# Kernel optimization log

Measured on AMD Instinct MI355X. Metric: run time of the kernel, lower is better.

## Reference

```python
import jax, jax.numpy as jnp
import numpy as np

B, L, DM = 8, 1024, 1024
H, P, N, K = 32, 64, 128, 4   # nheads, headdim, d_state, d_conv
DI = H * P                    # d_inner = expand * d_model = 2048
DXBC = DI + 2 * N             # conv channels = 2304
DINP = 2 * DI + 2 * N + H     # in_proj width = 4404
ED = 2048                     # embed_dim

def setup_inputs():
    key = jax.random.key(0)
    ks = jax.random.split(key, 10)
    s = lambda i, shape, scale=0.02: jax.random.normal(ks[i], shape, jnp.float32) * scale
    return {
        "bert_out": jax.random.normal(ks[0], (B, L, 1024), jnp.float32),
        "w_pb": s(1, (1024, DM)), "b_pb": jnp.zeros((DM,), jnp.float32),
        "w_in": s(2, (DM, DINP)),
        "conv_w": s(3, (DXBC, K), 0.2), "conv_b": jnp.zeros((DXBC,), jnp.float32),
        "dt_bias": jax.random.uniform(ks[4], (H,), jnp.float32, -4.0, 0.0),
        "A_log": jnp.log(jnp.arange(1, H + 1, dtype=jnp.float32)),
        "D": jnp.ones((H,), jnp.float32),
        "norm_w": jnp.ones((DI,), jnp.float32),
        "w_outp": s(5, (DI, DM)),
        "w_attn": s(6, (DM, 1)), "b_attn": jnp.zeros((1,), jnp.float32),
        "w_emb": s(7, (DM, ED)), "b_emb": jnp.zeros((ED,), jnp.float32),
    }

def reference(bert_out, w_pb, b_pb, w_in, conv_w, conv_b, dt_bias, A_log, D,
              norm_w, w_outp, w_attn, b_attn, w_emb, b_emb):
    x = bert_out @ w_pb + b_pb                          # [B,L,DM] proj_bert
    # ---- Mamba2 ----
    zxbcdt = x @ w_in                                   # [B,L,DINP]
    z, xBC, dt = jnp.split(zxbcdt, [DI, DI + DXBC], axis=-1)
    # causal depthwise conv1d (kernel K) + SiLU
    xp = jnp.pad(xBC, ((0, 0), (K - 1, 0), (0, 0)))
    xBC = sum(xp[:, k:k + L, :] * conv_w[:, k] for k in range(K)) + conv_b
    xBC = jax.nn.silu(xBC)
    xs, Bm, Cm = jnp.split(xBC, [DI, DI + N], axis=-1)  # [B,L,DI],[B,L,N],[B,L,N]
    xs = xs.reshape(B, L, H, P)
    dt = jax.nn.softplus(dt + dt_bias)                  # [B,L,H]
    dA = jnp.exp(dt * (-jnp.exp(A_log)))                # [B,L,H]
    def step(h, inp):
        dA_t, dt_t, B_t, C_t, x_t = inp
        h = h * dA_t[:, :, None, None] + jnp.einsum('bh,bn,bhp->bhpn', dt_t, B_t, x_t)
        return h, jnp.einsum('bhpn,bn->bhp', h, C_t)
    h0 = jnp.zeros((B, H, P, N), x.dtype)
    _, ys = jax.lax.scan(step, h0, (dA.transpose(1, 0, 2), dt.transpose(1, 0, 2),
                                    Bm.transpose(1, 0, 2), Cm.transpose(1, 0, 2),
                                    xs.transpose(1, 0, 2, 3)))
    y = ys.transpose(1, 0, 2, 3) + D[None, None, :, None] * xs   # skip term
    y = y.reshape(B, L, DI) * jax.nn.silu(z)                     # gated
    y = y * jax.lax.rsqrt(jnp.mean(y * y, axis=-1, keepdims=True) + 1e-5) * norm_w
    emb = y @ w_outp                                             # [B,L,DM]
    # ---- attention pooling ----
    w = jax.nn.softmax(emb @ w_attn + b_attn, axis=1)            # [B,L,1]
    pooled = (emb * w).sum(axis=1)                               # [B,DM]
    # dropout is identity in eval mode
    return pooled @ w_emb + b_emb                                # [B,ED]
```

## Files before the change

### kernel.cpp

```cpp
#include <hip/hip_runtime.h>
#include <hip/hip_bf16.h>
#include <math.h>

#define B_    8
#define L_    1024
#define DM_   1024
#define H_    32
#define P_    64
#define NS_   128
#define DI_   2048
#define DXBC_ 2304
#define DINP_ 4384
#define ED_   2048

typedef __attribute__((ext_vector_type(8))) short bf8_t;
typedef __attribute__((ext_vector_type(8))) unsigned short u16x8;
typedef __attribute__((ext_vector_type(4))) float f4_t;

__device__ __forceinline__ float silu_f(float x) { return x / (1.f + __expf(-x)); }

__device__ __forceinline__ unsigned short f2bf(float x) {
    unsigned u = __float_as_uint(x);
    unsigned r = u + 0x7fffu + ((u >> 16) & 1u);
    return (unsigned short)(r >> 16);
}
__device__ __forceinline__ float bf2f(unsigned short h) {
    return __uint_as_float(((unsigned)h) << 16);
}

__global__ __launch_bounds__(256) void convw_k(
    const float* __restrict__ W, unsigned short* __restrict__ hi,
    unsigned short* __restrict__ lo, int K, int N, int Npad)
{
    size_t e = (size_t)blockIdx.x * 256 + threadIdx.x;
    if (e >= (size_t)K * Npad) return;
    int n = (int)(e % Npad), k = (int)(e / Npad);
    float v = (n < N) ? W[(size_t)k * N + n] : 0.f;
    unsigned short h = f2bf(v);
    unsigned short l = f2bf(v - bf2f(h));
    int nt = n >> 7, r = n & 127, kt = k >> 5, c = k & 31;
    size_t dst = ((size_t)(nt * (K >> 5) + kt) << 12) + (r << 5) + c;
    hi[dst] = h; lo[dst] = l;
}

__global__ __launch_bounds__(256) void conva_k(
    const float* __restrict__ A, unsigned short* __restrict__ hi,
    unsigned short* __restrict__ lo, int M, int K)
{
    size_t e = (size_t)blockIdx.x * 256 + threadIdx.x;
    if (e >= (size_t)M * K) return;
    int k = (int)(e % K), m = (int)(e / K);
    float v = A[e];
    unsigned short h = f2bf(v);
    unsigned short l = f2bf(v - bf2f(h));
    int mt = m >> 7, r = m & 127, kt = k >> 5, c = k & 31;
    size_t dst = ((size_t)(mt * (K >> 5) + kt) << 12) + (r << 5) + c;
    hi[dst] = h; lo[dst] = l;
}

template<bool CHECK_N>
__global__ __launch_bounds__(256, 2) void bgemm_k(
    const unsigned short* __restrict__ Ahi, const unsigned short* __restrict__ Alo,
    const unsigned short* __restrict__ Whi, const unsigned short* __restrict__ Wlo,
    float* __restrict__ C, const float* __restrict__ bias, int N, int K, int ldc)
{
    __shared__ unsigned short Ah[128 * 40], Al[128 * 40];
    __shared__ unsigned short Bh[128 * 40], Bl[128 * 40];
    const int tid = threadIdx.x;
    const int m0 = blockIdx.y * 128, n0 = blockIdx.x * 128;
    const int lane = tid & 63;
    const int wv = tid >> 6;
    const int wr = wv >> 1, wc = wv & 1;
    const int l15 = lane & 15, l4 = lane >> 4;
    const int KT = K >> 5;

    f4_t acc[4][4];
#pragma unroll
    for (int i = 0; i < 4; i++)
#pragma unroll
        for (int j = 0; j < 4; j++) acc[i][j] = (f4_t){0.f, 0.f, 0.f, 0.f};

    const int trow = tid >> 1;
    const int tcol = (tid & 1) * 16;
    const int soff = trow * 40 + tcol;

    u16x8 rAh0, rAh1, rAl0, rAl1, rWh0, rWh1, rWl0, rWl1;
#define LOADKT(KTI) {                                                               \
        size_t aoff = (((size_t)(blockIdx.y * KT + (KTI))) << 12) + (trow << 5) + tcol; \
        size_t woff = (((size_t)(blockIdx.x * KT + (KTI))) << 12) + (trow << 5) + tcol; \
        rAh0 = *(const u16x8*)(Ahi + aoff); rAh1 = *(const u16x8*)(Ahi + aoff + 8); \
        rAl0 = *(const u16x8*)(Alo + aoff); rAl1 = *(const u16x8*)(Alo + aoff + 8); \
        rWh0 = *(const u16x8*)(Whi + woff); rWh1 = *(const u16x8*)(Whi + woff + 8); \
        rWl0 = *(const u16x8*)(Wlo + woff); rWl1 = *(const u16x8*)(Wlo + woff + 8); }

    LOADKT(0);
    for (int kt = 0; kt < KT; ++kt) {
        __syncthreads();
        *(u16x8*)&Ah[soff]     = rAh0;
        *(u16x8*)&Ah[soff + 8] = rAh1;
        *(u16x8*)&Al[soff]     = rAl0;
        *(u16x8*)&Al[soff + 8] = rAl1;
        *(u16x8*)&Bh[soff]     = rWh0;
        *(u16x8*)&Bh[soff + 8] = rWh1;
        *(u16x8*)&Bl[soff]     = rWl0;
        *(u16x8*)&Bl[soff + 8] = rWl1;
        __syncthreads();
        if (kt + 1 < KT) LOADKT(kt + 1);

        bf8_t afh[4], afl[4], bfh[4], bfl[4];
#pragma unroll
        for (int i = 0; i < 4; i++) {
            int off = (wr * 64 + i * 16 + l15) * 40 + l4 * 8;
            afh[i] = *(const bf8_t*)&Ah[off];
            afl[i] = *(const bf8_t*)&Al[off];
        }
#pragma unroll
        for (int j = 0; j < 4; j++) {
            int off = (wc * 64 + j * 16 + l15) * 40 + l4 * 8;
            bfh[j] = *(const bf8_t*)&Bh[off];
            bfl[j] = *(const bf8_t*)&Bl[off];
        }
#pragma unroll
        for (int i = 0; i < 4; i++)
#pragma unroll
            for (int j = 0; j < 4; j++) {
                acc[i][j] = __builtin_amdgcn_mfma_f32_16x16x32_bf16(afh[i], bfh[j], acc[i][j], 0, 0, 0);
                acc[i][j] = __builtin_amdgcn_mfma_f32_16x16x32_bf16(afl[i], bfh[j], acc[i][j], 0, 0, 0);
                acc[i][j] = __builtin_amdgcn_mfma_f32_16x16x32_bf16(afh[i], bfl[j], acc[i][j], 0, 0, 0);
            }
    }
#undef LOADKT

#pragma unroll
    for (int j = 0; j < 4; j++) {
        int col = n0 + wc * 64 + j * 16 + l15;
        bool ok = !CHECK_N || (col < N);
        float bv = 0.f;
        if (bias && ok) bv = bias[col];
        if (ok) {
#pragma unroll
            for (int i = 0; i < 4; i++) {
                int rbase = m0 + wr * 64 + i * 16 + l4 * 4;
#pragma unroll
                for (int r = 0; r < 4; r++)
                    C[(size_t)(rbase + r) * ldc + col] = acc[i][j][r] + bv;
            }
        }
    }
}

template<bool CHECK_N>
__global__ __launch_bounds__(256, 2) void sgemm_k(
    const float* __restrict__ A, const float* __restrict__ Bw,
    float* __restrict__ C, const float* __restrict__ bias,
    int M, int N, int K, int ldb, int ldc)
{
    __shared__ float As[16][128];
    __shared__ float Bs[16][128];
    const int tid = threadIdx.x;
    const int m0 = blockIdx.y * 128;
    const int n0 = blockIdx.x * 128;
    const int tx = tid & 15;
    const int ty = tid >> 4;
    const int arr = tid >> 1;
    const int acc_ = (tid & 1) * 8;
    const int bk = tid >> 5;
    const int bn = (tid & 31) * 4;

    float acc[8][8];
#pragma unroll
    for (int i = 0; i < 8; i++)
#pragma unroll
        for (int j = 0; j < 8; j++) acc[i][j] = 0.f;

    for (int k0 = 0; k0 < K; k0 += 16) {
        float4 a0 = *(const float4*)(A + (size_t)(m0 + arr) * K + k0 + acc_);
        float4 a1 = *(const float4*)(A + (size_t)(m0 + arr) * K + k0 + acc_ + 4);
        float4 b0, b1;
        if (!CHECK_N || (n0 + bn) < N) {
            b0 = *(const float4*)(Bw + (size_t)(k0 + bk) * ldb + n0 + bn);
            b1 = *(const float4*)(Bw + (size_t)(k0 + bk + 8) * ldb + n0 + bn);
        } else {
            b0 = make_float4(0.f, 0.f, 0.f, 0.f);
            b1 = make_float4(0.f, 0.f, 0.f, 0.f);
        }
        __syncthreads();
        As[acc_ + 0][arr] = a0.x; As[acc_ + 1][arr] = a0.y;
        As[acc_ + 2][arr] = a0.z; As[acc_ + 3][arr] = a0.w;
        As[acc_ + 4][arr] = a1.x; As[acc_ + 5][arr] = a1.y;
        As[acc_ + 6][arr] = a1.z; As[acc_ + 7][arr] = a1.w;
        *(float4*)&Bs[bk][bn]     = b0;
        *(float4*)&Bs[bk + 8][bn] = b1;
        __syncthreads();
#pragma unroll
        for (int kk = 0; kk < 16; kk++) {
            float4 av0 = *(const float4*)&As[kk][ty * 8];
            float4 av1 = *(const float4*)&As[kk][ty * 8 + 4];
            float4 bv0 = *(const float4*)&Bs[kk][tx * 4];
            float4 bv1 = *(const float4*)&Bs[kk][64 + tx * 4];
            float a_[8] = {av0.x, av0.y, av0.z, av0.w, av1.x, av1.y, av1.z, av1.w};
            float b_[8] = {bv0.x, bv0.y, bv0.z, bv0.w, bv1.x, bv1.y, bv1.z, bv1.w};
#pragma unroll
            for (int i = 0; i < 8; i++)
#pragma unroll
                for (int j = 0; j < 8; j++) acc[i][j] += a_[i] * b_[j];
        }
    }
    float4 bb0 = make_float4(0.f, 0.f, 0.f, 0.f), bb1 = bb0;
    if (bias) {
        if (!CHECK_N || (n0 + tx * 4) < N)      bb0 = *(const float4*)(bias + n0 + tx * 4);
        if (!CHECK_N || (n0 + 64 + tx * 4) < N) bb1 = *(const float4*)(bias + n0 + 64 + tx * 4);
    }
#pragma unroll
    for (int i = 0; i < 8; i++) {
        size_t row = (size_t)(m0 + ty * 8 + i) * ldc + n0;
        if (!CHECK_N || (n0 + tx * 4) < N) {
            float4 v = make_float4(acc[i][0] + bb0.x, acc[i][1] + bb0.y,
                                   acc[i][2] + bb0.z, acc[i][3] + bb0.w);
            *(float4*)(C + row + tx * 4) = v;
        }
        if (!CHECK_N || (n0 + 64 + tx * 4) < N) {
            float4 v = make_float4(acc[i][4] + bb1.x, acc[i][5] + bb1.y,
                                   acc[i][6] + bb1.z, acc[i][7] + bb1.w);
            *(float4*)(C + row + 64 + tx * 4) = v;
        }
    }
}

__global__ __launch_bounds__(256) void dt_k(
    const float* __restrict__ zx, const float* __restrict__ dt_bias,
    const float* __restrict__ A_log, float* __restrict__ dtp, float* __restrict__ dAb)
{
    int e = blockIdx.x * 256 + threadIdx.x;
    int l = e & 1023;
    int h = (e >> 10) & 31;
    int b = e >> 15;
    float dtr = zx[((size_t)b * L_ + l) * DINP_ + (DI_ + DXBC_) + h];
    float u = dtr + dt_bias[h];
    float sp = (u > 20.f) ? u : log1pf(__expf(u));
    float da = __expf(-__expf(A_log[h]) * sp);
    size_t o = ((size_t)b * H_ + h) * L_ + l;
    dtp[o] = sp;
    dAb[o] = da;
}

__global__ __launch_bounds__(256) void stash_k(const float* __restrict__ zx, float* __restrict__ stash)
{
    int e = blockIdx.x * 256 + threadIdx.x;
    int c = e % DXBC_;
    int r = e / DXBC_;
    int k = r % 3;
    int bc = r / 3;
    int chunk = bc & 7;
    int b = bc >> 3;
    int t = chunk * 128 - 3 + k;
    float v = 0.f;
    if (t >= 0) v = zx[((size_t)b * L_ + t) * DINP_ + DI_ + c];
    stash[e] = v;
}

__global__ __launch_bounds__(256) void conv_k(
    float* __restrict__ zx, const float* __restrict__ cw,
    const float* __restrict__ cb, const float* __restrict__ stash)
{
    int tid = threadIdx.x;
    int cblk = blockIdx.x;
    int chunk = blockIdx.y;
    int b = blockIdx.z;
    int c = cblk * 256 + tid;
    float4 w = *(const float4*)(cw + (size_t)c * 4);
    float bias = cb[c];
    const float* st = stash + ((size_t)(b * 8 + chunk) * 3) * DXBC_ + c;
    float x0 = st[0], x1 = st[DXBC_], x2 = st[2 * DXBC_];
    int t0 = chunk * 128;
    size_t base = ((size_t)b * L_ + t0) * DINP_ + DI_ + c;
#pragma unroll 4
    for (int t = 0; t < 128; t++) {
        float xt = zx[base + (size_t)t * DINP_];
        float a = w.x * x0 + w.y * x1 + w.z * x2 + w.w * xt + bias;
        a = a / (1.f + __expf(-a));
        zx[base + (size_t)t * DINP_] = a;
        x0 = x1; x1 = x2; x2 = xt;
    }
}

__global__ __launch_bounds__(1024, 1) void scan_k(
    const float* __restrict__ zx, const float* __restrict__ dtp,
    const float* __restrict__ dAb, const float* __restrict__ Dp,
    float* __restrict__ ys)
{
    int bh = blockIdx.x;
    int b = bh >> 5, h = bh & 31;
    int tid = threadIdx.x;
    int lane = tid & 63;
    int gu = __builtin_amdgcn_readfirstlane(tid >> 6);
    int nbase = gu * 8;
    __shared__ float ypart[8][16][64];
    __shared__ float bcs[8][256];
    __shared__ float xss[8][64];
    __shared__ float dtda[2][8];
    float hreg[8];
#pragma unroll
    for (int j = 0; j < 8; j++) hreg[j] = 0.f;
    float Dh = Dp[h];
    const float* dtrow = dtp + ((size_t)b * H_ + h) * L_;
    const float* darow = dAb + ((size_t)b * H_ + h) * L_;

    const int st_t = tid >> 7;
    const int st_j = (tid & 127) * 2;
    const int sx_t = tid >> 6;
    const int sx_ok = (sx_t < 8);

    {
        size_t row = ((size_t)b * L_ + st_t) * DINP_;
        float2 bc2 = *(const float2*)(zx + row + 2 * DI_ + st_j);
        *(float2*)&bcs[st_t][st_j] = bc2;
        if (sx_ok) {
            size_t rowx = ((size_t)b * L_ + sx_t) * DINP_;
            xss[sx_t][lane] = zx[rowx + DI_ + h * 64 + lane];
        }
        if (tid < 8)               dtda[0][tid] = dtrow[tid];
        else if (tid < 16)         dtda[1][tid - 8] = darow[tid - 8];
    }
    __syncthreads();

    float xout = 0.f;
    for (int c0 = 0; c0 < L_; c0 += 8) {
        float2 nbc; float nx = 0.f, nd = 0.f;
        const bool pf = (c0 + 8) < L_;
        if (pf) {
            size_t row = ((size_t)b * L_ + c0 + 8 + st_t) * DINP_;
            nbc = *(const float2*)(zx + row + 2 * DI_ + st_j);
            if (sx_ok) {
                size_t rowx = ((size_t)b * L_ + c0 + 8 + sx_t) * DINP_;
                nx = zx[rowx + DI_ + h * 64 + lane];
            }
            if (tid < 8)       nd = dtrow[c0 + 8 + tid];
            else if (tid < 16) nd = darow[c0 + 8 + tid - 8];
        }
#pragma unroll
        for (int tt = 0; tt < 8; ++tt) {
            float dtv = dtda[0][tt];
            float dav = dtda[1][tt];
            float xv  = xss[tt][lane];
            if (tt == gu) xout = xv;
            float4 b0  = *(const float4*)&bcs[tt][nbase];
            float4 b1  = *(const float4*)&bcs[tt][nbase + 4];
            float4 cv0 = *(const float4*)&bcs[tt][128 + nbase];
            float4 cv1 = *(const float4*)&bcs[tt][128 + nbase + 4];
            float u = dtv * xv;
            float ya = 0.f, yb = 0.f;
            hreg[0] = hreg[0] * dav + u * b0.x; ya += hreg[0] * cv0.x;
            hreg[1] = hreg[1] * dav + u * b0.y; yb += hreg[1] * cv0.y;
            hreg[2] = hreg[2] * dav + u * b0.z; ya += hreg[2] * cv0.z;
            hreg[3] = hreg[3] * dav + u * b0.w; yb += hreg[3] * cv0.w;
            hreg[4] = hreg[4] * dav + u * b1.x; ya += hreg[4] * cv1.x;
            hreg[5] = hreg[5] * dav + u * b1.y; yb += hreg[5] * cv1.y;
            hreg[6] = hreg[6] * dav + u * b1.z; ya += hreg[6] * cv1.z;
            hreg[7] = hreg[7] * dav + u * b1.w; yb += hreg[7] * cv1.w;
            ypart[tt][gu][lane] = ya + yb;
        }
        __syncthreads();
        if (gu < 8) {
            int t = c0 + gu;
            float v = 0.f;
#pragma unroll
            for (int w = 0; w < 16; w++) v += ypart[gu][w][lane];
            ys[((size_t)b * L_ + t) * DI_ + h * 64 + lane] = v + Dh * xout;
        }
        if (pf) {
            *(float2*)&bcs[st_t][st_j] = nbc;
            if (sx_ok) xss[sx_t][lane] = nx;
            if (tid < 8)       dtda[0][tid] = nd;
            else if (tid < 16) dtda[1][tid - 8] = nd;
        }
        __syncthreads();
    }
}

__global__ __launch_bounds__(256) void gate_norm_k(
    float* __restrict__ ys, const float* __restrict__ zx, const float* __restrict__ nw)
{
    int row = blockIdx.x;
    int tid = threadIdx.x;
    float* yr = ys + (size_t)row * DI_;
    const float* zr = zx + (size_t)row * DINP_;
    float4 v[2];
    float ss = 0.f;
#pragma unroll
    for (int i = 0; i < 2; i++) {
        int d = tid * 4 + i * 1024;
        float4 yv = *(const float4*)(yr + d);
        float4 zv = *(const float4*)(zr + d);
        v[i].x = yv.x * silu_f(zv.x);
        v[i].y = yv.y * silu_f(zv.y);
        v[i].z = yv.z * silu_f(zv.z);
        v[i].w = yv.w * silu_f(zv.w);
        ss += v[i].x * v[i].x + v[i].y * v[i].y + v[i].z * v[i].z + v[i].w * v[i].w;
    }
    __shared__ float red[256];
    red[tid] = ss;
    __syncthreads();
    for (int s = 128; s > 0; s >>= 1) {
        if (tid < s) red[tid] += red[tid + s];
        __syncthreads();
    }
    float scale = rsqrtf(red[0] / (float)DI_ + 1e-5f);
#pragma unroll
    for (int i = 0; i < 2; i++) {
        int d = tid * 4 + i * 1024;
        float4 nwv = *(const float4*)(nw + d);
        float4 o = make_float4(v[i].x * scale * nwv.x, v[i].y * scale * nwv.y,
                               v[i].z * scale * nwv.z, v[i].w * scale * nwv.w);
        *(float4*)(yr + d) = o;
    }
}

__global__ __launch_bounds__(256) void attnw_k(
    const float* __restrict__ emb, const float* __restrict__ wat,
    const float* __restrict__ batn, float* __restrict__ logits)
{
    int row = blockIdx.x * 4 + (threadIdx.x >> 6);
    int lane = threadIdx.x & 63;
    const float* er = emb + (size_t)row * DM_;
    float s = 0.f;
#pragma unroll
    for (int k = 0; k < 16; k++) s += er[lane + k * 64] * wat[lane + k * 64];
#pragma unroll
    for (int off = 32; off; off >>= 1) s += __shfl_down(s, off);
    if (lane == 0) logits[row] = s + batn[0];
}

__global__ __launch_bounds__(256) void softmax_k(
    const float* __restrict__ logits, float* __restrict__ wght, float* __restrict__ pooled)
{
    int b = blockIdx.x;
    int tid = threadIdx.x;
    __shared__ float red[256];
    float4 lv = *(const float4*)(logits + (size_t)b * L_ + tid * 4);
    float m = fmaxf(fmaxf(lv.x, lv.y), fmaxf(lv.z, lv.w));
    red[tid] = m;
    __syncthreads();
    for (int s = 128; s > 0; s >>= 1) {
        if (tid < s) red[tid] = fmaxf(red[tid], red[tid + s]);
        __syncthreads();
    }
    float bm = red[0];
    __syncthreads();
    float e0 = __expf(lv.x - bm), e1 = __expf(lv.y - bm);
    float e2 = __expf(lv.z - bm), e3 = __expf(lv.w - bm);
    red[tid] = e0 + e1 + e2 + e3;
    __syncthreads();
    for (int s = 128; s > 0; s >>= 1) {
        if (tid < s) red[tid] += red[tid + s];
        __syncthreads();
    }
    float inv = 1.f / red[0];
    *(float4*)(wght + (size_t)b * L_ + tid * 4) = make_float4(e0 * inv, e1 * inv, e2 * inv, e3 * inv);
    *(float4*)(pooled + (size_t)b * DM_ + tid * 4) = make_float4(0.f, 0.f, 0.f, 0.f);
}

__global__ __launch_bounds__(256) void pool_k(
    const float* __restrict__ emb, const float* __restrict__ wght, float* __restrict__ pooled)
{
    int b = blockIdx.x, dc = blockIdx.y, lc = blockIdx.z;
    int d = dc * 256 + threadIdx.x;
    const float* wr = wght + (size_t)b * L_ + lc * 64;
    float acc = 0.f;
#pragma unroll 4
    for (int lt = 0; lt < 64; lt++)
        acc += emb[((size_t)(b * L_ + lc * 64 + lt)) * DM_ + d] * wr[lt];
    atomicAdd(pooled + (size_t)b * DM_ + d, acc);
}

__global__ __launch_bounds__(256) void outp_k(
    const float* __restrict__ pooled, const float* __restrict__ wemb,
    const float* __restrict__ bemb, float* __restrict__ out)
{
    int ec = blockIdx.x, b = blockIdx.y;
    int tid = threadIdx.x;
    __shared__ float pl[DM_];
#pragma unroll
    for (int i = 0; i < 4; i++) pl[tid + i * 256] = pooled[(size_t)b * DM_ + tid + i * 256];
    __syncthreads();
    int e = ec * 256 + tid;
    float acc = bemb[e];
#pragma unroll 4
    for (int d = 0; d < DM_; d++) acc += pl[d] * wemb[(size_t)d * ED_ + e];
    out[(size_t)b * ED_ + e] = acc;
}

extern "C" void kernel_launch(void* const* d_in, const int* in_sizes, int n_in,
                              void* d_out, int out_size, void* d_ws, size_t ws_size,
                              hipStream_t stream)
{
    (void)in_sizes; (void)n_in; (void)out_size;
    const float* bert    = (const float*)d_in[0];
    const float* w_pb    = (const float*)d_in[1];
    const float* b_pb    = (const float*)d_in[2];
    const float* w_in    = (const float*)d_in[3];
    const float* conv_w  = (const float*)d_in[4];
    const float* conv_b  = (const float*)d_in[5];
    const float* dt_bias = (const float*)d_in[6];
    const float* A_log   = (const float*)d_in[7];
    const float* Dp      = (const float*)d_in[8];
    const float* norm_w  = (const float*)d_in[9];
    const float* w_outp  = (const float*)d_in[10];
    const float* w_attn  = (const float*)d_in[11];
    const float* b_attn  = (const float*)d_in[12];
    const float* w_emb   = (const float*)d_in[13];
    const float* b_emb   = (const float*)d_in[14];
    float* out = (float*)d_out;

    float* ws     = (float*)d_ws;
    float* zx     = ws;
    float* ys     = zx  + (size_t)8192 * 4384;
    float* xe     = ys  + (size_t)8192 * 2048;
    float* dtp    = xe  + (size_t)8192 * 1024;
    float* dAb    = dtp + 262144;
    float* stash  = dAb + 262144;
    float* logits = stash + 442368;
    float* wght   = logits + 8192;
    float* pooled = wght + 8192;
    float* fend   = pooled + 8192;

    size_t wpb_n = (size_t)8  * 32 * 4096;
    size_t win_n = (size_t)35 * 32 * 4096;
    size_t wop_n = (size_t)8  * 64 * 4096;
    size_t aT_n  = (size_t)64 * 32 * 4096;
    size_t ysT_n = (size_t)64 * 64 * 4096;
    unsigned short* wpb_h = (unsigned short*)ys;
    unsigned short* wpb_l = wpb_h + wpb_n;
    unsigned short* win_h = wpb_l + wpb_n;
    unsigned short* win_l = win_h + win_n;
    unsigned short* aT_h  = win_l + win_n;
    unsigned short* aT_l  = aT_h + aT_n;
    unsigned short* wop_h = (unsigned short*)zx;
    unsigned short* wop_l = wop_h + wop_n;
    unsigned short* ysT_h = (unsigned short*)zx + 6291456;
    unsigned short* ysT_l = ysT_h + ysT_n;

    size_t need_bytes = (size_t)((char*)fend - (char*)d_ws);
    bool use_mfma = ws_size >= need_bytes;

    if (use_mfma) {
        convw_k<<<(unsigned)(((size_t)1024 * 1024 + 255) / 256), 256, 0, stream>>>(
            w_pb, wpb_h, wpb_l, 1024, 1024, 1024);
        convw_k<<<(unsigned)(((size_t)1024 * 4480 + 255) / 256), 256, 0, stream>>>(
            w_in, win_h, win_l, 1024, 4384, 4480);
        conva_k<<<32768, 256, 0, stream>>>(bert, aT_h, aT_l, 8192, 1024);
        bgemm_k<false><<<dim3(8, 64), 256, 0, stream>>>(aT_h, aT_l, wpb_h, wpb_l,
                                                        xe, b_pb, 1024, 1024, 1024);
        conva_k<<<32768, 256, 0, stream>>>(xe, aT_h, aT_l, 8192, 1024);
        bgemm_k<true><<<dim3(35, 64), 256, 0, stream>>>(aT_h, aT_l, win_h, win_l,
                                                        zx, nullptr, 4384, 1024, 4384);
    } else {
        sgemm_k<false><<<dim3(8, 64), 256, 0, stream>>>(bert, w_pb, xe, b_pb,
                                                        8192, 1024, 1024, 1024, 1024);
        sgemm_k<true><<<dim3(35, 64), 256, 0, stream>>>(xe, w_in, zx, nullptr,
                                                        8192, 4384, 1024, 4384, 4384);
    }
    dt_k<<<1024, 256, 0, stream>>>(zx, dt_bias, A_log, dtp, dAb);
    stash_k<<<1728, 256, 0, stream>>>(zx, stash);
    conv_k<<<dim3(9, 8, 8), 256, 0, stream>>>(zx, conv_w, conv_b, stash);
    scan_k<<<256, 1024, 0, stream>>>(zx, dtp, dAb, Dp, ys);
    gate_norm_k<<<8192, 256, 0, stream>>>(ys, zx, norm_w);
    if (use_mfma) {
        convw_k<<<(unsigned)(((size_t)2048 * 1024 + 255) / 256), 256, 0, stream>>>(
            w_outp, wop_h, wop_l, 2048, 1024, 1024);
        conva_k<<<65536, 256, 0, stream>>>(ys, ysT_h, ysT_l, 8192, 2048);
        bgemm_k<false><<<dim3(8, 64), 256, 0, stream>>>(ysT_h, ysT_l, wop_h, wop_l,
                                                        xe, nullptr, 1024, 2048, 1024);
    } else {
        sgemm_k<false><<<dim3(8, 64), 256, 0, stream>>>(ys, w_outp, xe, nullptr,
                                                        8192, 1024, 2048, 1024, 1024);
    }
    attnw_k<<<2048, 256, 0, stream>>>(xe, w_attn, b_attn, logits);
    softmax_k<<<8, 256, 0, stream>>>(logits, wght, pooled);
    pool_k<<<dim3(8, 4, 16), 256, 0, stream>>>(xe, wght, pooled);
    outp_k<<<dim3(8, 8), 256, 0, stream>>>(pooled, w_emb, b_emb, out);
}
```

Before: 1.022 ms.

## Fuse bf16 hi/lo activation splitting into GEMM epilogue and prologue

The first GEMM now writes its output directly in the tiled bf16 hi/lo layout, so the separate conva_k pass over xe before the in_proj GEMM is gone. The out_proj GEMM gets a new kernel that reads fp32 activations and does the hi/lo split while staging into shared memory, which removes the conva_k pass over ys. Both changes cut full-tensor round trips through global memory. The cost is extra conversion ALU work and scattered 2-byte stores in the epilogue, and the conversion now sits inside the GEMM main loop.

```diff
diff --git a/kernel.cpp b/kernel.cpp
--- a/kernel.cpp
+++ b/kernel.cpp
@@ -58,11 +58,13 @@
     hi[dst] = h; lo[dst] = l;
 }
 
-template<bool CHECK_N>
-__global__ __launch_bounds__(256, 2) void bgemm_k(
+template<bool TILED_OUT, bool CHECK_N>
+__global__ __launch_bounds__(256, 2) void bgemm_pt(
     const unsigned short* __restrict__ Ahi, const unsigned short* __restrict__ Alo,
     const unsigned short* __restrict__ Whi, const unsigned short* __restrict__ Wlo,
-    float* __restrict__ C, const float* __restrict__ bias, int N, int K, int ldc)
+    float* __restrict__ C, unsigned short* __restrict__ Ohi,
+    unsigned short* __restrict__ Olo, const float* __restrict__ bias,
+    int N, int K, int ldc)
 {
     __shared__ unsigned short Ah[128 * 40], Al[128 * 40];
     __shared__ unsigned short Bh[128 * 40], Bl[128 * 40];
@@ -137,7 +139,23 @@
         bool ok = !CHECK_N || (col < N);
         float bv = 0.f;
         if (bias && ok) bv = bias[col];
-        if (ok) {
+        if (!ok) continue;
+        if (TILED_OUT) {
+            int kt2 = col >> 5, c2 = col & 31;
+            size_t tbase = (((size_t)(blockIdx.y * (N >> 5) + kt2)) << 12) + c2;
+#pragma unroll
+            for (int i = 0; i < 4; i++) {
+                int rbase = wr * 64 + i * 16 + l4 * 4;
+#pragma unroll
+                for (int r = 0; r < 4; r++) {
+                    float v = acc[i][j][r] + bv;
+                    unsigned short hh = f2bf(v);
+                    unsigned short ll = f2bf(v - bf2f(hh));
+                    size_t dst = tbase + ((size_t)(rbase + r) << 5);
+                    Ohi[dst] = hh; Olo[dst] = ll;
+                }
+            }
+        } else {
 #pragma unroll
             for (int i = 0; i < 4; i++) {
                 int rbase = m0 + wr * 64 + i * 16 + l4 * 4;
@@ -145,6 +163,108 @@
                 for (int r = 0; r < 4; r++)
                     C[(size_t)(rbase + r) * ldc + col] = acc[i][j][r] + bv;
             }
+        }
+    }
+}
+
+__global__ __launch_bounds__(256, 2) void bgemm_fa(
+    const float* __restrict__ A, const unsigned short* __restrict__ Whi,
+    const unsigned short* __restrict__ Wlo, float* __restrict__ C,
+    const float* __restrict__ bias, int N, int K, int ldc)
+{
+    __shared__ unsigned short Ah[128 * 40], Al[128 * 40];
+    __shared__ unsigned short Bh[128 * 40], Bl[128 * 40];
+    const int tid = threadIdx.x;
+    const int m0 = blockIdx.y * 128, n0 = blockIdx.x * 128;
+    const int lane = tid & 63;
+    const int wv = tid >> 6;
+    const int wr = wv >> 1, wc = wv & 1;
+    const int l15 = lane & 15, l4 = lane >> 4;
+    const int KT = K >> 5;
+
+    f4_t acc[4][4];
+#pragma unroll
+    for (int i = 0; i < 4; i++)
+#pragma unroll
+        for (int j = 0; j < 4; j++) acc[i][j] = (f4_t){0.f, 0.f, 0.f, 0.f};
+
+    const int ar = tid >> 2;
+    const int ac = (tid & 3) * 8;
+    const int trow = tid >> 1;
+    const int tcol = (tid & 1) * 16;
+    const int soff = trow * 40 + tcol;
+
+    float4 a00, a01, a10, a11;
+    u16x8 rWh0, rWh1, rWl0, rWl1;
+#define LOADKT(KTI) {                                                               \
+        const float* Ap0 = A + (size_t)(m0 + ar) * K + (KTI) * 32 + ac;             \
+        const float* Ap1 = Ap0 + (size_t)64 * K;                                    \
+        a00 = *(const float4*)Ap0; a01 = *(const float4*)(Ap0 + 4);                 \
+        a10 = *(const float4*)Ap1; a11 = *(const float4*)(Ap1 + 4);                 \
+        size_t woff = (((size_t)(blockIdx.x * KT + (KTI))) << 12) + (trow << 5) + tcol; \
+        rWh0 = *(const u16x8*)(Whi + woff); rWh1 = *(const u16x8*)(Whi + woff + 8); \
+        rWl0 = *(const u16x8*)(Wlo + woff); rWl1 = *(const u16x8*)(Wlo + woff + 8); }
+
+    LOADKT(0);
+    for (int kt = 0; kt < KT; ++kt) {
+        __syncthreads();
+        {
+            float av0[8] = {a00.x, a00.y, a00.z, a00.w, a01.x, a01.y, a01.z, a01.w};
+            float av1[8] = {a10.x, a10.y, a10.z, a10.w, a11.x, a11.y, a11.z, a11.w};
+            u16x8 vh0, vl0, vh1, vl1;
+#pragma unroll
+            for (int j = 0; j < 8; j++) {
+                unsigned short h0 = f2bf(av0[j]);
+                vh0[j] = h0; vl0[j] = f2bf(av0[j] - bf2f(h0));
+                unsigned short h1 = f2bf(av1[j]);
+                vh1[j] = h1; vl1[j] = f2bf(av1[j] - bf2f(h1));
+            }
+            *(u16x8*)&Ah[ar * 40 + ac] = vh0;
+            *(u16x8*)&Al[ar * 40 + ac] = vl0;
+            *(u16x8*)&Ah[(ar + 64) * 40 + ac] = vh1;
+            *(u16x8*)&Al[(ar + 64) * 40 + ac] = vl1;
+            *(u16x8*)&Bh[soff]     = rWh0;
+            *(u16x8*)&Bh[soff + 8] = rWh1;
+            *(u16x8*)&Bl[soff]     = rWl0;
+            *(u16x8*)&Bl[soff + 8] = rWl1;
+        }
+        __syncthreads();
+        if (kt + 1 < KT) LOADKT(kt + 1);
+
+        bf8_t afh[4], afl[4], bfh[4], bfl[4];
+#pragma unroll
+        for (int i = 0; i < 4; i++) {
+            int off = (wr * 64 + i * 16 + l15) * 40 + l4 * 8;
+            afh[i] = *(const bf8_t*)&Ah[off];
+            afl[i] = *(const bf8_t*)&Al[off];
+        }
+#pragma unroll
+        for (int j = 0; j < 4; j++) {
+            int off = (wc * 64 + j * 16 + l15) * 40 + l4 * 8;
+            bfh[j] = *(const bf8_t*)&Bh[off];
+            bfl[j] = *(const bf8_t*)&Bl[off];
+        }
+#pragma unroll
+        for (int i = 0; i < 4; i++)
+#pragma unroll
+            for (int j = 0; j < 4; j++) {
+                acc[i][j] = __builtin_amdgcn_mfma_f32_16x16x32_bf16(afh[i], bfh[j], acc[i][j], 0, 0, 0);
+                acc[i][j] = __builtin_amdgcn_mfma_f32_16x16x32_bf16(afl[i], bfh[j], acc[i][j], 0, 0, 0);
+                acc[i][j] = __builtin_amdgcn_mfma_f32_16x16x32_bf16(afh[i], bfl[j], acc[i][j], 0, 0, 0);
+            }
+    }
+#undef LOADKT
+
+#pragma unroll
+    for (int j = 0; j < 4; j++) {
+        int col = n0 + wc * 64 + j * 16 + l15;
+        float bv = bias ? bias[col] : 0.f;
+#pragma unroll
+        for (int i = 0; i < 4; i++) {
+            int rbase = m0 + wr * 64 + i * 16 + l4 * 4;
+#pragma unroll
+            for (int r = 0; r < 4; r++)
+                C[(size_t)(rbase + r) * ldc + col] = acc[i][j][r] + bv;
         }
     }
 }
@@ -524,21 +644,20 @@
     float* pooled = wght + 8192;
     float* fend   = pooled + 8192;
 
-    size_t wpb_n = (size_t)8  * 32 * 4096;
-    size_t win_n = (size_t)35 * 32 * 4096;
-    size_t wop_n = (size_t)8  * 64 * 4096;
-    size_t aT_n  = (size_t)64 * 32 * 4096;
-    size_t ysT_n = (size_t)64 * 64 * 4096;
-    unsigned short* wpb_h = (unsigned short*)ys;
-    unsigned short* wpb_l = wpb_h + wpb_n;
-    unsigned short* win_h = wpb_l + wpb_n;
-    unsigned short* win_l = win_h + win_n;
-    unsigned short* aT_h  = win_l + win_n;
-    unsigned short* aT_l  = aT_h + aT_n;
-    unsigned short* wop_h = (unsigned short*)zx;
-    unsigned short* wop_l = wop_h + wop_n;
-    unsigned short* ysT_h = (unsigned short*)zx + 6291456;
-    unsigned short* ysT_l = ysT_h + ysT_n;
+    size_t wpb_n  = (size_t)8  * 32 * 4096;
+    size_t win_n  = (size_t)35 * 32 * 4096;
+    size_t wop_n  = (size_t)8  * 64 * 4096;
+    size_t aT_n   = (size_t)64 * 32 * 4096;
+    unsigned short* wpb_h  = (unsigned short*)ys;
+    unsigned short* wpb_l  = wpb_h + wpb_n;
+    unsigned short* win_h  = wpb_l + wpb_n;
+    unsigned short* win_l  = win_h + win_n;
+    unsigned short* xeT_h  = win_l + win_n;
+    unsigned short* xeT_l  = xeT_h + aT_n;
+    unsigned short* bertT_h = (unsigned short*)zx;
+    unsigned short* bertT_l = bertT_h + aT_n;
+    unsigned short* wop_h  = (unsigned short*)zx;
+    unsigned short* wop_l  = wop_h + wop_n;
 
     size_t need_bytes = (size_t)((char*)fend - (char*)d_ws);
     bool use_mfma = ws_size >= need_bytes;
@@ -548,12 +667,13 @@
             w_pb, wpb_h, wpb_l, 1024, 1024, 1024);
         convw_k<<<(unsigned)(((size_t)1024 * 4480 + 255) / 256), 256, 0, stream>>>(
             w_in, win_h, win_l, 1024, 4384, 4480);
-        conva_k<<<32768, 256, 0, stream>>>(bert, aT_h, aT_l, 8192, 1024);
-        bgemm_k<false><<<dim3(8, 64), 256, 0, stream>>>(aT_h, aT_l, wpb_h, wpb_l,
-                                                        xe, b_pb, 1024, 1024, 1024);
-        conva_k<<<32768, 256, 0, stream>>>(xe, aT_h, aT_l, 8192, 1024);
-        bgemm_k<true><<<dim3(35, 64), 256, 0, stream>>>(aT_h, aT_l, win_h, win_l,
-                                                        zx, nullptr, 4384, 1024, 4384);
+        conva_k<<<32768, 256, 0, stream>>>(bert, bertT_h, bertT_l, 8192, 1024);
+        bgemm_pt<true, false><<<dim3(8, 64), 256, 0, stream>>>(
+            bertT_h, bertT_l, wpb_h, wpb_l, nullptr, xeT_h, xeT_l, b_pb,
+            1024, 1024, 0);
+        bgemm_pt<false, true><<<dim3(35, 64), 256, 0, stream>>>(
+            xeT_h, xeT_l, win_h, win_l, zx, nullptr, nullptr, nullptr,
+            4384, 1024, 4384);
     } else {
         sgemm_k<false><<<dim3(8, 64), 256, 0, stream>>>(bert, w_pb, xe, b_pb,
                                                         8192, 1024, 1024, 1024, 1024);
@@ -568,9 +688,8 @@
     if (use_mfma) {
         convw_k<<<(unsigned)(((size_t)2048 * 1024 + 255) / 256), 256, 0, stream>>>(
             w_outp, wop_h, wop_l, 2048, 1024, 1024);
-        conva_k<<<65536, 256, 0, stream>>>(ys, ysT_h, ysT_l, 8192, 2048);
-        bgemm_k<false><<<dim3(8, 64), 256, 0, stream>>>(ysT_h, ysT_l, wop_h, wop_l,
-                                                        xe, nullptr, 1024, 2048, 1024);
+        bgemm_fa<<<dim3(8, 64), 256, 0, stream>>>(ys, wop_h, wop_l, xe, nullptr,
+                                                  1024, 2048, 1024);
     } else {
         sgemm_k<false><<<dim3(8, 64), 256, 0, stream>>>(ys, w_outp, xe, nullptr,
                                                         8192, 1024, 2048, 1024, 1024);
```

Result: faster. 985.1 us (-3.6%).
